# Kernel tuning notes

Measured on AMD Instinct MI355X. Metric: run time of the kernel, lower is better.

Reference implementation:

```python
import jax, jax.numpy as jnp
import numpy as np

B, N, IN, OUT, H, F = 4, 2048, 128, 64, 4, 64


def setup_inputs() -> dict:
    key = jax.random.key(0)
    ks = jax.random.split(key, 10)
    h = jax.random.normal(ks[0], (B, N, IN), dtype=jnp.float32)
    projection_matrix = jax.random.uniform(ks[1], (B, N, N), dtype=jnp.float32)
    similarity_matrix = jnp.tanh(jax.random.normal(ks[2], (B, N, N), dtype=jnp.float32))
    quadrant_matrix = jax.random.randint(ks[3], (B, N, N, 2), 0, 4)
    # learned params (xavier-ish scaling); stored as (in, out) so x @ W
    W = jax.random.normal(ks[4], (IN, OUT * H), dtype=jnp.float32) * (1.0 / np.sqrt(IN))
    random_projection = jax.random.normal(ks[5], (IN, F), dtype=jnp.float32) * 0.1
    a_q = jax.random.normal(ks[6], (2 * F, OUT), dtype=jnp.float32) * (1.0 / np.sqrt(2 * F))
    a_k = jax.random.normal(ks[7], (2 * F, OUT), dtype=jnp.float32) * (1.0 / np.sqrt(2 * F))
    quadrant_bias = jax.random.normal(ks[8], (4, 4), dtype=jnp.float32) * 0.02
    output_proj = jax.random.normal(ks[9], (OUT * H, OUT), dtype=jnp.float32) * (1.0 / np.sqrt(OUT * H))
    return {
        "h": h,
        "projection_matrix": projection_matrix,
        "similarity_matrix": similarity_matrix,
        "W": W,
        "random_projection": random_projection,
        "a_q": a_q,
        "a_k": a_k,
        "quadrant_bias": quadrant_bias,
        "output_proj": output_proj,
        "quadrant_matrix": quadrant_matrix,
    }


def reference(h, projection_matrix, similarity_matrix, W, random_projection,
              a_q, a_k, quadrant_bias, output_proj, quadrant_matrix):
    # random feature map: phi = [cos(h R), sin(h R)]  -> (B, N, 2F)
    proj = jnp.einsum('bnd,df->bnf', h, random_projection)
    phi = jnp.concatenate([jnp.cos(proj), jnp.sin(proj)], axis=-1)
    Q = phi @ a_q                       # (B, N, OUT)
    K = phi @ a_k                       # (B, N, OUT)
    Wh = (h @ W).reshape(h.shape[0], h.shape[1], H, OUT)  # (B, N, H, OUT)

    scores = jnp.einsum('bio,bjo->bij', Q, K)             # (B, N, N)
    # additive relational biases (shared across heads)
    qb = quadrant_bias[quadrant_matrix[..., 0], quadrant_matrix[..., 1]]  # (B, N, N)
    scores = scores + projection_matrix + similarity_matrix + qb
    attn = jax.nn.softmax(scores[:, None, :, :], axis=-1)  # (B, H, N, N) via broadcast

    # aggregate values per head, then concat heads
    hp = jnp.einsum('bhij,bjhk->bihk', attn, Wh)           # (B, N, H, OUT)
    hp = hp.reshape(h.shape[0], h.shape[1], H * OUT)
    out = hp @ output_proj                                  # (B, N, OUT)
    return jax.nn.elu(out)
```

## Files before the change

kernel.cpp:

```cpp
#include <hip/hip_runtime.h>
#include <math.h>

#define BB   4
#define NN   2048
#define IND  128
#define CDIM 256
#define NIT  16

typedef _Float16 half_t;
typedef _Float16 half4_t __attribute__((ext_vector_type(4)));
typedef _Float16 half8_t __attribute__((ext_vector_type(8)));
typedef float    f32x4   __attribute__((ext_vector_type(4)));

#define SHIFT 16.0f

__global__ __launch_bounds__(256) void precompute_kernel(
    const float* __restrict__ hg,
    const float* __restrict__ W,
    const float* __restrict__ R,
    const float* __restrict__ aq,
    const float* __restrict__ ak,
    half_t* __restrict__ Qw,
    half_t* __restrict__ Kw,
    half_t* __restrict__ WhJ)
{
    const int tid  = threadIdx.x;
    const int row0 = blockIdx.x * 8;

    __shared__ float hs[8][IND];
    __shared__ float phis[8][IND];

    {
        const float4* src = (const float4*)(hg + (size_t)row0 * IND);
        ((float4*)&hs[0][0])[tid] = src[tid];
    }
    __syncthreads();

    {
        const int f  = tid & 63;
        const int rr = tid >> 6;
        float p0 = 0.f, p1 = 0.f;
        #pragma unroll 4
        for (int d0 = 0; d0 < IND; d0 += 4) {
            const float r0 = R[(d0 + 0) * 64 + f];
            const float r1 = R[(d0 + 1) * 64 + f];
            const float r2 = R[(d0 + 2) * 64 + f];
            const float r3 = R[(d0 + 3) * 64 + f];
            const float4 ha = *(const float4*)&hs[rr][d0];
            const float4 hb = *(const float4*)&hs[rr + 4][d0];
            p0 += ha.x * r0 + ha.y * r1 + ha.z * r2 + ha.w * r3;
            p1 += hb.x * r0 + hb.y * r1 + hb.z * r2 + hb.w * r3;
        }
        float s, c;
        __sincosf(p0, &s, &c); phis[rr][f]     = c; phis[rr][f + 64]     = s;
        __sincosf(p1, &s, &c); phis[rr + 4][f] = c; phis[rr + 4][f + 64] = s;
    }

    {
        float acc[8];
        #pragma unroll
        for (int r = 0; r < 8; ++r) acc[r] = 0.f;
        #pragma unroll 2
        for (int d0 = 0; d0 < IND; d0 += 4) {
            const float w0 = W[(d0 + 0) * CDIM + tid];
            const float w1 = W[(d0 + 1) * CDIM + tid];
            const float w2 = W[(d0 + 2) * CDIM + tid];
            const float w3 = W[(d0 + 3) * CDIM + tid];
            #pragma unroll
            for (int r = 0; r < 8; ++r) {
                const float4 h4 = *(const float4*)&hs[r][d0];
                acc[r] += h4.x * w0 + h4.y * w1 + h4.z * w2 + h4.w * w3;
            }
        }
        const int b   = row0 >> 11;
        const int j16 = (row0 & (NN - 1)) >> 4;
        const int jr0 = row0 & 8;
        half8_t v;
        #pragma unroll
        for (int r = 0; r < 8; ++r) v[r] = (half_t)acc[r];
        *(half8_t*)(WhJ + (((size_t)b * 128 + j16) * CDIM + tid) * 16 + jr0) = v;
    }
    __syncthreads();

    {
        const int o  = tid & 63;
        const int qk = (tid >> 6) & 1;
        const int rh = tid >> 7;
        const float* A = qk ? ak : aq;
        half_t*    Dst = qk ? Kw : Qw;
        float acc[4] = {0.f, 0.f, 0.f, 0.f};
        #pragma unroll 2
        for (int t0 = 0; t0 < IND; t0 += 4) {
            const float a0 = A[(t0 + 0) * 64 + o];
            const float a1 = A[(t0 + 1) * 64 + o];
            const float a2 = A[(t0 + 2) * 64 + o];
            const float a3 = A[(t0 + 3) * 64 + o];
            #pragma unroll
            for (int r = 0; r < 4; ++r) {
                const float4 ph = *(const float4*)&phis[rh * 4 + r][t0];
                acc[r] += ph.x * a0 + ph.y * a1 + ph.z * a2 + ph.w * a3;
            }
        }
        #pragma unroll
        for (int r = 0; r < 4; ++r)
            Dst[(size_t)(row0 + rh * 4 + r) * 64 + o] = (half_t)acc[r];
    }
}

#define ITER5(IT, KC0, KC1, KN0, KN1, PB)                                       \
  {                                                                             \
       \
    const half_t* wpt = wb + (size_t)(IT) * (8 * CDIM * 16);                    \
    half4_t bwv[16];                                                            \
    _Pragma("unroll")                                                           \
    for (int kk = 0; kk < 8; ++kk) {                                            \
      bwv[2 * kk]     = *(const half4_t*)(wpt + (size_t)kk * (CDIM * 16));      \
      bwv[2 * kk + 1] = *(const half4_t*)(wpt + (size_t)kk * (CDIM * 16) + 256);\
    }                                                                           \
            \
    if ((IT) + 1 < NIT) {                                                       \
      half4_t hb;                                                               \
      hb[0] = (half_t)(pmv.x + smv.x + qbs[(qiv0.x << 2) | qiv0.y]);            \
      hb[1] = (half_t)(pmv.y + smv.y + qbs[(qiv0.z << 2) | qiv0.w]);            \
      hb[2] = (half_t)(pmv.z + smv.z + qbs[(qiv1.x << 2) | qiv1.y]);            \
      hb[3] = (half_t)(pmv.w + smv.w + qbs[(qiv1.z << 2) | qiv1.w]);            \
      *(half4_t*)&Bl[1 - (PB)][str][stc] = hb;                                  \
    }                                                                           \
                                  \
    if ((IT) + 2 < NIT) {                                                       \
      pmv  = *(const float4*)(pmt + ((IT) + 2) * 128);                          \
      smv  = *(const float4*)(smt + ((IT) + 2) * 128);                          \
      qiv0 = *(const int4*)(qmt + (size_t)((IT) + 2) * 256);                    \
      qiv1 = *(const int4*)(qmt + (size_t)((IT) + 2) * 256 + 4);                \
    }                                                                           \
                                     \
    f32x4 s4 = (f32x4){0.f, 0.f, 0.f, 0.f};                                     \
    s4 = __builtin_amdgcn_mfma_f32_16x16x32_f16(KC0, qf0, s4, 0, 0, 0);         \
    s4 = __builtin_amdgcn_mfma_f32_16x16x32_f16(KC1, qf1, s4, 0, 0, 0);         \
    if ((IT) + 1 < NIT) {                                                       \
      const half_t* kp = kbase + (size_t)((IT) + 1) * 128 * 64;                 \
      KN0 = *(const half8_t*)(kp + q * 8);                                      \
      KN1 = *(const half8_t*)(kp + 32 + q * 8);                                 \
    }                                                                           \
          \
    const half4_t bh = *(const half4_t*)&Bl[PB][n][cbase];                      \
    const float sv0 = s4[0] + (float)bh[0] - SHIFT;                             \
    const float sv1 = s4[1] + (float)bh[1] - SHIFT;                             \
    const float sv2 = s4[2] + (float)bh[2] - SHIFT;                             \
    const float sv3 = s4[3] + (float)bh[3] - SHIFT;                             \
    const half_t h0 = (half_t)__expf(fminf(sv0, 11.f));                         \
    const half_t h1 = (half_t)__expf(fminf(sv1, 11.f));                         \
    const half_t h2 = (half_t)__expf(fminf(sv2, 11.f));                         \
    const half_t h3 = (half_t)__expf(fminf(sv3, 11.f));                         \
    half4_t aP; aP[0] = h0; aP[1] = h1; aP[2] = h2; aP[3] = h3;                 \
    lacc += (float)h0 + (float)h1 + (float)h2 + (float)h3;                      \
    *(half4_t*)&Pl[PB][w][lane * 4] = aP;                                       \
    asm volatile("s_waitcnt lgkmcnt(0)" ::: "memory");                          \
    __builtin_amdgcn_s_barrier();                                               \
    asm volatile("" ::: "memory");                                              \
                 \
    _Pragma("unroll")                                                           \
    for (int kk = 0; kk < 8; ++kk) {                                            \
      const half4_t pa = *(const half4_t*)&Pl[PB][kk][lane * 4];                \
      acc0 = __builtin_amdgcn_mfma_f32_16x16x16f16(pa, bwv[2 * kk],     acc0, 0, 0, 0); \
      acc1 = __builtin_amdgcn_mfma_f32_16x16x16f16(pa, bwv[2 * kk + 1], acc1, 0, 0, 0); \
    }                                                                           \
  }

__global__ __launch_bounds__(512, 4) void attn5_kernel(
    const half_t* __restrict__ Qw, const half_t* __restrict__ Kw,
    const half_t* __restrict__ WhJ,
    const float* __restrict__ pm,
    const float* __restrict__ sm,
    const int*   __restrict__ qm,
    const float* __restrict__ qbias,
    const float* __restrict__ op,
    float* __restrict__ out)
{
    const int tid  = threadIdx.x;
    const int w    = tid >> 6;
    const int lane = tid & 63;
    const int n    = lane & 15;
    const int q    = lane >> 4;

    const int blk = blockIdx.x;
    const int b   = (blk & 7) >> 1;
    const int i0  = (((blk >> 3) << 1) | (blk & 1)) * 16;

    __shared__ __align__(16) half_t Pl[2][8][256];
    __shared__ __align__(16) half_t Bl[2][16][132];
    __shared__ __align__(16) float  BufT0[CDIM][20];
    __shared__ float Lp[8][16];
    __shared__ float qbs[16];

    if (tid < 16) qbs[tid] = qbias[tid];

    const half_t* qptr = Qw + ((size_t)(b * NN) + i0 + n) * 64;
    const half8_t qf0 = *(const half8_t*)(qptr + q * 8);
    const half8_t qf1 = *(const half8_t*)(qptr + 32 + q * 8);

    const int str = tid >> 5;
    const int stc = (tid & 31) * 4;
    const float* pmt = pm + ((size_t)b * NN + i0 + str) * NN + stc;
    const float* smt = sm + ((size_t)b * NN + i0 + str) * NN + stc;
    const int*   qmt = qm + (((size_t)b * NN + i0 + str) * NN + stc) * 2;

    const int cbase = w * 16 + q * 4;

    const half_t* kbase = Kw + ((size_t)b * NN + w * 16 + n) * 64;
    const half_t* wb = WhJ + ((size_t)b * 128 * CDIM + (size_t)(w * 32 + n)) * 16 + q * 4;

    float4 pmv  = *(const float4*)(pmt);
    float4 smv  = *(const float4*)(smt);
    int4   qiv0 = *(const int4*)(qmt);
    int4   qiv1 = *(const int4*)(qmt + 4);
    half8_t ka0 = *(const half8_t*)(kbase + q * 8);
    half8_t ka1 = *(const half8_t*)(kbase + 32 + q * 8);
    half8_t kb0 = ka0, kb1 = ka1;
    __syncthreads();
    {
        half4_t hb;
        hb[0] = (half_t)(pmv.x + smv.x + qbs[(qiv0.x << 2) | qiv0.y]);
        hb[1] = (half_t)(pmv.y + smv.y + qbs[(qiv0.z << 2) | qiv0.w]);
        hb[2] = (half_t)(pmv.z + smv.z + qbs[(qiv1.x << 2) | qiv1.y]);
        hb[3] = (half_t)(pmv.w + smv.w + qbs[(qiv1.z << 2) | qiv1.w]);
        *(half4_t*)&Bl[0][str][stc] = hb;
    }
    pmv  = *(const float4*)(pmt + 128);
    smv  = *(const float4*)(smt + 128);
    qiv0 = *(const int4*)(qmt + 256);
    qiv1 = *(const int4*)(qmt + 256 + 4);
    __syncthreads();

    f32x4 acc0 = (f32x4){0.f, 0.f, 0.f, 0.f};
    f32x4 acc1 = (f32x4){0.f, 0.f, 0.f, 0.f};
    float lacc = 0.f;

    for (int it = 0; it < NIT; it += 2) {
        ITER5(it,     ka0, ka1, kb0, kb1, 0)
        ITER5(it + 1, kb0, kb1, ka0, ka1, 1)
    }

    lacc += __shfl_xor(lacc, 16);
    lacc += __shfl_xor(lacc, 32);
    if (lane < 16) Lp[w][lane] = lacc;

    *(f32x4*)&BufT0[w * 32 + n][q * 4]      = acc0;
    *(f32x4*)&BufT0[w * 32 + 16 + n][q * 4] = acc1;
    __syncthreads();

    {
        const int r0 = 2 * w, r1 = 2 * w + 1;
        float pacc0 = 0.f, pacc1 = 0.f;
        #pragma unroll 8
        for (int c = 0; c < CDIM; ++c) {
            const float wv = op[c * 64 + lane];
            pacc0 += BufT0[c][r0] * wv;
            pacc1 += BufT0[c][r1] * wv;
        }
        float lt0 = 0.f, lt1 = 0.f;
        #pragma unroll
        for (int gg = 0; gg < 8; ++gg) { lt0 += Lp[gg][r0]; lt1 += Lp[gg][r1]; }
        float x0 = pacc0 / lt0;
        float x1 = pacc1 / lt1;
        x0 = x0 > 0.f ? x0 : (__expf(x0) - 1.f);
        x1 = x1 > 0.f ? x1 : (__expf(x1) - 1.f);
        out[((size_t)b * NN + i0 + r0) * 64 + lane] = x0;
        out[((size_t)b * NN + i0 + r1) * 64 + lane] = x1;
    }
}

extern "C" void kernel_launch(void* const* d_in, const int* in_sizes, int n_in,
                              void* d_out, int out_size, void* d_ws, size_t ws_size,
                              hipStream_t stream) {
    (void)in_sizes; (void)n_in; (void)out_size; (void)ws_size;
    const float* h  = (const float*)d_in[0];
    const float* pm = (const float*)d_in[1];
    const float* sm = (const float*)d_in[2];
    const float* W  = (const float*)d_in[3];
    const float* R  = (const float*)d_in[4];
    const float* aq = (const float*)d_in[5];
    const float* ak = (const float*)d_in[6];
    const float* qb = (const float*)d_in[7];
    const float* op = (const float*)d_in[8];
    const int*   qm = (const int*)d_in[9];
    float* out = (float*)d_out;

    half_t* ws  = (half_t*)d_ws;
    half_t* Qw  = ws;
    half_t* Kw  = ws + (size_t)BB * NN * 64;
    half_t* WhJ = ws + (size_t)BB * NN * 64 * 2;

    precompute_kernel<<<BB * NN / 8, 256, 0, stream>>>(h, W, R, aq, ak, Qw, Kw, WhJ);
    attn5_kernel<<<BB * (NN / 16), 512, 0, stream>>>(Qw, Kw, WhJ, pm, sm, qm, qb, op, out);
}
```

Baseline: 337.7 us.

## Prefetch bias tiles four iterations ahead with grouped staging and aliased LDS

The bias staging for projection, similarity and quadrant inputs now loads and fuses four 128-column tiles per group of four iterations, one group ahead, instead of one tile two iterations ahead. The fuse work is spread across the group's iterations. This gives the global loads of the large N×N bias matrices more time in flight and hides their latency. The shared memory is merged into one aliased buffer, with the epilogue buffer reusing the bias region, so LDS use per block stays low at four blocks per CU. The cost is more registers held for the staged loads, which risks spills or lower occupancy.

```diff
diff --git a/kernel.cpp b/kernel.cpp
--- a/kernel.cpp
+++ b/kernel.cpp
@@ -107,32 +107,56 @@
     }
 }
 
-#define ITER5(IT, KC0, KC1, KN0, KN1, PB)                                       \
+#define BLI(gb, k, r, c) ((gb) * 8448 + (k) * 2112 + (r) * 132 + (c))
+
+#define STG_NONE
+
+#define STG_A(G)                                                                \
+    _Pragma("unroll")                                                           \
+    for (int k2 = 0; k2 < 4; ++k2) {                                            \
+      s_pm[k2] = *(const float4*)(pmt + ((G) + 1) * 512 + k2 * 128);            \
+      s_sm[k2] = *(const float4*)(smt + ((G) + 1) * 512 + k2 * 128);            \
+    }                                                                           \
+    _Pragma("unroll")                                                           \
+    for (int k2 = 0; k2 < 2; ++k2) {                                            \
+      s_qA[2*k2]   = *(const int4*)(qmt + (size_t)((((G)+1)*512 + k2*128) * 2));     \
+      s_qA[2*k2+1] = *(const int4*)(qmt + (size_t)((((G)+1)*512 + k2*128) * 2 + 4)); \
+    }
+
+#define STG_FUSE(G, KOFF, QARR)                                                 \
+    _Pragma("unroll")                                                           \
+    for (int k2 = 0; k2 < 2; ++k2) {                                            \
+      const float4 fp = s_pm[k2 + (KOFF)], fs = s_sm[k2 + (KOFF)];              \
+      const int4 ia = QARR[2*k2], ib = QARR[2*k2+1];                            \
+      half4_t hbv;                                                              \
+      hbv[0] = (half_t)(fp.x + fs.x + qbs[(ia.x << 2) | ia.y]);                 \
+      hbv[1] = (half_t)(fp.y + fs.y + qbs[(ia.z << 2) | ia.w]);                 \
+      hbv[2] = (half_t)(fp.z + fs.z + qbs[(ib.x << 2) | ib.y]);                 \
+      hbv[3] = (half_t)(fp.w + fs.w + qbs[(ib.z << 2) | ib.w]);                 \
+      *(half4_t*)&Blp[BLI((((G) + 1) & 1), k2 + (KOFF), str, stc)] = hbv;       \
+    }
+
+#define STG_B(G)                                                                \
+    STG_FUSE(G, 0, s_qA)                                                        \
+    _Pragma("unroll")                                                           \
+    for (int k2 = 0; k2 < 2; ++k2) {                                            \
+      s_qB[2*k2]   = *(const int4*)(qmt + (size_t)((((G)+1)*512 + (k2+2)*128) * 2));     \
+      s_qB[2*k2+1] = *(const int4*)(qmt + (size_t)((((G)+1)*512 + (k2+2)*128) * 2 + 4)); \
+    }
+
+#define STG_C(G)  STG_FUSE(G, 2, s_qB)
+
+#define ITER6(IT, KC0, KC1, KN0, KN1, PB, GB, KK, STAGE)                        \
   {                                                                             \
        \
     const half_t* wpt = wb + (size_t)(IT) * (8 * CDIM * 16);                    \
     half4_t bwv[16];                                                            \
     _Pragma("unroll")                                                           \
-    for (int kk = 0; kk < 8; ++kk) {                                            \
-      bwv[2 * kk]     = *(const half4_t*)(wpt + (size_t)kk * (CDIM * 16));      \
-      bwv[2 * kk + 1] = *(const half4_t*)(wpt + (size_t)kk * (CDIM * 16) + 256);\
+    for (int kq = 0; kq < 8; ++kq) {                                            \
+      bwv[2 * kq]     = *(const half4_t*)(wpt + (size_t)kq * (CDIM * 16));      \
+      bwv[2 * kq + 1] = *(const half4_t*)(wpt + (size_t)kq * (CDIM * 16) + 256);\
     }                                                                           \
-            \
-    if ((IT) + 1 < NIT) {                                                       \
-      half4_t hb;                                                               \
-      hb[0] = (half_t)(pmv.x + smv.x + qbs[(qiv0.x << 2) | qiv0.y]);            \
-      hb[1] = (half_t)(pmv.y + smv.y + qbs[(qiv0.z << 2) | qiv0.w]);            \
-      hb[2] = (half_t)(pmv.z + smv.z + qbs[(qiv1.x << 2) | qiv1.y]);            \
-      hb[3] = (half_t)(pmv.w + smv.w + qbs[(qiv1.z << 2) | qiv1.w]);            \
-      *(half4_t*)&Bl[1 - (PB)][str][stc] = hb;                                  \
-    }                                                                           \
-                                  \
-    if ((IT) + 2 < NIT) {                                                       \
-      pmv  = *(const float4*)(pmt + ((IT) + 2) * 128);                          \
-      smv  = *(const float4*)(smt + ((IT) + 2) * 128);                          \
-      qiv0 = *(const int4*)(qmt + (size_t)((IT) + 2) * 256);                    \
-      qiv1 = *(const int4*)(qmt + (size_t)((IT) + 2) * 256 + 4);                \
-    }                                                                           \
+    STAGE                                                                       \
                                      \
     f32x4 s4 = (f32x4){0.f, 0.f, 0.f, 0.f};                                     \
     s4 = __builtin_amdgcn_mfma_f32_16x16x32_f16(KC0, qf0, s4, 0, 0, 0);         \
@@ -142,8 +166,8 @@
       KN0 = *(const half8_t*)(kp + q * 8);                                      \
       KN1 = *(const half8_t*)(kp + 32 + q * 8);                                 \
     }                                                                           \
-          \
-    const half4_t bh = *(const half4_t*)&Bl[PB][n][cbase];                      \
+                    \
+    const half4_t bh = *(const half4_t*)&Blp[BLI(GB, KK, n, cbase)];            \
     const float sv0 = s4[0] + (float)bh[0] - SHIFT;                             \
     const float sv1 = s4[1] + (float)bh[1] - SHIFT;                             \
     const float sv2 = s4[2] + (float)bh[2] - SHIFT;                             \
@@ -154,20 +178,20 @@
     const half_t h3 = (half_t)__expf(fminf(sv3, 11.f));                         \
     half4_t aP; aP[0] = h0; aP[1] = h1; aP[2] = h2; aP[3] = h3;                 \
     lacc += (float)h0 + (float)h1 + (float)h2 + (float)h3;                      \
-    *(half4_t*)&Pl[PB][w][lane * 4] = aP;                                       \
+    *(half4_t*)&Pl[(PB) * 2048 + w * 256 + lane * 4] = aP;                      \
     asm volatile("s_waitcnt lgkmcnt(0)" ::: "memory");                          \
     __builtin_amdgcn_s_barrier();                                               \
     asm volatile("" ::: "memory");                                              \
                  \
     _Pragma("unroll")                                                           \
-    for (int kk = 0; kk < 8; ++kk) {                                            \
-      const half4_t pa = *(const half4_t*)&Pl[PB][kk][lane * 4];                \
-      acc0 = __builtin_amdgcn_mfma_f32_16x16x16f16(pa, bwv[2 * kk],     acc0, 0, 0, 0); \
-      acc1 = __builtin_amdgcn_mfma_f32_16x16x16f16(pa, bwv[2 * kk + 1], acc1, 0, 0, 0); \
+    for (int kq = 0; kq < 8; ++kq) {                                            \
+      const half4_t pa = *(const half4_t*)&Pl[(PB) * 2048 + kq * 256 + lane * 4]; \
+      acc0 = __builtin_amdgcn_mfma_f32_16x16x16f16(pa, bwv[2 * kq],     acc0, 0, 0, 0); \
+      acc1 = __builtin_amdgcn_mfma_f32_16x16x16f16(pa, bwv[2 * kq + 1], acc1, 0, 0, 0); \
     }                                                                           \
   }
 
-__global__ __launch_bounds__(512, 4) void attn5_kernel(
+__global__ __launch_bounds__(512, 4) void attn6_kernel(
     const half_t* __restrict__ Qw, const half_t* __restrict__ Kw,
     const half_t* __restrict__ WhJ,
     const float* __restrict__ pm,
@@ -187,13 +211,12 @@
     const int b   = (blk & 7) >> 1;
     const int i0  = (((blk >> 3) << 1) | (blk & 1)) * 16;
 
-    __shared__ __align__(16) half_t Pl[2][8][256];
-    __shared__ __align__(16) half_t Bl[2][16][132];
-    __shared__ __align__(16) float  BufT0[CDIM][20];
-    __shared__ float Lp[8][16];
-    __shared__ float qbs[16];
-
-    if (tid < 16) qbs[tid] = qbias[tid];
+    __shared__ __align__(16) unsigned char smem[42560];
+    half_t* const Blp = (half_t*)(smem + 8192);
+    half_t* const Pl  = (half_t*)smem;
+    float*  const Buf = (float*)(smem + 8192);
+    float*  const Lp  = (float*)(smem + 41984);
+    float*  const qbs = (float*)(smem + 42496);
 
     const half_t* qptr = Qw + ((size_t)(b * NN) + i0 + n) * 64;
     const half8_t qf0 = *(const half8_t*)(qptr + q * 8);
@@ -210,43 +233,55 @@
     const half_t* kbase = Kw + ((size_t)b * NN + w * 16 + n) * 64;
     const half_t* wb = WhJ + ((size_t)b * 128 * CDIM + (size_t)(w * 32 + n)) * 16 + q * 4;
 
-    float4 pmv  = *(const float4*)(pmt);
-    float4 smv  = *(const float4*)(smt);
-    int4   qiv0 = *(const int4*)(qmt);
-    int4   qiv1 = *(const int4*)(qmt + 4);
+    float4 s_pm[4], s_sm[4];
+    int4   s_qA[4], s_qB[4];
+    #pragma unroll
+    for (int k2 = 0; k2 < 4; ++k2) {
+        s_pm[k2] = *(const float4*)(pmt + k2 * 128);
+        s_sm[k2] = *(const float4*)(smt + k2 * 128);
+    }
+    #pragma unroll
+    for (int k2 = 0; k2 < 2; ++k2) {
+        s_qA[2*k2]   = *(const int4*)(qmt + (size_t)((k2 * 128) * 2));
+        s_qA[2*k2+1] = *(const int4*)(qmt + (size_t)((k2 * 128) * 2 + 4));
+        s_qB[2*k2]   = *(const int4*)(qmt + (size_t)(((k2 + 2) * 128) * 2));
+        s_qB[2*k2+1] = *(const int4*)(qmt + (size_t)(((k2 + 2) * 128) * 2 + 4));
+    }
     half8_t ka0 = *(const half8_t*)(kbase + q * 8);
     half8_t ka1 = *(const half8_t*)(kbase + 32 + q * 8);
     half8_t kb0 = ka0, kb1 = ka1;
-    __syncthreads();
-    {
-        half4_t hb;
-        hb[0] = (half_t)(pmv.x + smv.x + qbs[(qiv0.x << 2) | qiv0.y]);
-        hb[1] = (half_t)(pmv.y + smv.y + qbs[(qiv0.z << 2) | qiv0.w]);
-        hb[2] = (half_t)(pmv.z + smv.z + qbs[(qiv1.x << 2) | qiv1.y]);
-        hb[3] = (half_t)(pmv.w + smv.w + qbs[(qiv1.z << 2) | qiv1.w]);
-        *(half4_t*)&Bl[0][str][stc] = hb;
-    }
-    pmv  = *(const float4*)(pmt + 128);
-    smv  = *(const float4*)(smt + 128);
-    qiv0 = *(const int4*)(qmt + 256);
-    qiv1 = *(const int4*)(qmt + 256 + 4);
+    if (tid < 16) qbs[tid] = qbias[tid];
+    __syncthreads();
+    STG_FUSE(-1, 0, s_qA)
+    STG_FUSE(-1, 2, s_qB)
     __syncthreads();
 
     f32x4 acc0 = (f32x4){0.f, 0.f, 0.f, 0.f};
     f32x4 acc1 = (f32x4){0.f, 0.f, 0.f, 0.f};
     float lacc = 0.f;
 
-    for (int it = 0; it < NIT; it += 2) {
-        ITER5(it,     ka0, ka1, kb0, kb1, 0)
-        ITER5(it + 1, kb0, kb1, ka0, ka1, 1)
+    #pragma unroll
+    for (int g = 0; g < 4; ++g) {
+        const int gb = g & 1;
+        if (g < 3) {
+            ITER6(4*g + 0, ka0, ka1, kb0, kb1, 0, gb, 0, STG_A(g))
+            ITER6(4*g + 1, kb0, kb1, ka0, ka1, 1, gb, 1, STG_B(g))
+            ITER6(4*g + 2, ka0, ka1, kb0, kb1, 0, gb, 2, STG_C(g))
+            ITER6(4*g + 3, kb0, kb1, ka0, ka1, 1, gb, 3, STG_NONE)
+        } else {
+            ITER6(4*g + 0, ka0, ka1, kb0, kb1, 0, gb, 0, STG_NONE)
+            ITER6(4*g + 1, kb0, kb1, ka0, ka1, 1, gb, 1, STG_NONE)
+            ITER6(4*g + 2, ka0, ka1, kb0, kb1, 0, gb, 2, STG_NONE)
+            ITER6(4*g + 3, kb0, kb1, ka0, ka1, 1, gb, 3, STG_NONE)
+        }
     }
 
     lacc += __shfl_xor(lacc, 16);
     lacc += __shfl_xor(lacc, 32);
-    if (lane < 16) Lp[w][lane] = lacc;
-
-    *(f32x4*)&BufT0[w * 32 + n][q * 4]      = acc0;
-    *(f32x4*)&BufT0[w * 32 + 16 + n][q * 4] = acc1;
+    if (lane < 16) Lp[w * 16 + lane] = lacc;
+
+    *(f32x4*)&Buf[(w * 32 + n) * 20 + q * 4]      = acc0;
+    *(f32x4*)&Buf[(w * 32 + 16 + n) * 20 + q * 4] = acc1;
     __syncthreads();
 
     {
@@ -255,12 +290,12 @@
         #pragma unroll 8
         for (int c = 0; c < CDIM; ++c) {
             const float wv = op[c * 64 + lane];
-            pacc0 += BufT0[c][r0] * wv;
-            pacc1 += BufT0[c][r1] * wv;
+            pacc0 += Buf[c * 20 + r0] * wv;
+            pacc1 += Buf[c * 20 + r1] * wv;
         }
         float lt0 = 0.f, lt1 = 0.f;
         #pragma unroll
-        for (int gg = 0; gg < 8; ++gg) { lt0 += Lp[gg][r0]; lt1 += Lp[gg][r1]; }
+        for (int gg = 0; gg < 8; ++gg) { lt0 += Lp[gg * 16 + r0]; lt1 += Lp[gg * 16 + r1]; }
         float x0 = pacc0 / lt0;
         float x1 = pacc1 / lt1;
         x0 = x0 > 0.f ? x0 : (__expf(x0) - 1.f);
@@ -292,5 +327,5 @@
     half_t* WhJ = ws + (size_t)BB * NN * 64 * 2;
 
     precompute_kernel<<<BB * NN / 8, 256, 0, stream>>>(h, W, R, aq, ak, Qw, Kw, WhJ);
-    attn5_kernel<<<BB * (NN / 16), 512, 0, stream>>>(Qw, Kw, WhJ, pm, sm, qm, qb, op, out);
+    attn6_kernel<<<BB * (NN / 16), 512, 0, stream>>>(Qw, Kw, WhJ, pm, sm, qm, qb, op, out);
 }
```

Measured after the change: 382.0 us. +13.1%, slower.
